# Performance work log

Hardware: AMD Instinct MI355X
Metric: run time of the kernel (lower is better)

## Reference

```python
import jax, jax.numpy as jnp
import numpy as np

ALPHA = 2.0  # snntorch ATan surrogate default (irrelevant for fwd-only)


def _spike(x):
    return (x > 0).astype(x.dtype)


def setup_inputs() -> dict:
    key = jax.random.key(0)
    ks = jax.random.split(key, 7)
    B, T, H, O = 2048, 120, 512, 2
    sample_rate = 40.0
    x = jax.random.normal(ks[0], (B, T), dtype=jnp.float32)
    # fc1: [H, 1], fc2: [O, H] (torch Linear weight layout), gaussian init near 1/sample_rate scale
    W1 = (1.0 / sample_rate) + (0.5 / sample_rate) * jax.random.normal(ks[1], (H, 1), dtype=jnp.float32)
    W2 = (1.0 / (sample_rate * H)) + (0.5 / (sample_rate * H)) * jax.random.normal(ks[2], (O, H), dtype=jnp.float32)
    W2 = W2 * H  # keep output currents at a useful magnitude
    beta_h = 0.8 + 0.19 * jax.random.uniform(ks[3], (H,), dtype=jnp.float32)
    thr_h = 1.0 + 0.1 * jax.random.uniform(ks[4], (H,), dtype=jnp.float32)
    beta_o = 0.8 + 0.19 * jax.random.uniform(ks[5], (O,), dtype=jnp.float32)
    thr_o = 1.0 + 0.1 * jax.random.uniform(ks[6], (O,), dtype=jnp.float32)
    return {"x": x, "W1": W1, "W2": W2, "beta_h": beta_h, "thr_h": thr_h,
            "beta_o": beta_o, "thr_o": thr_o}


def reference(x, W1, W2, beta_h, thr_h, beta_o, thr_o):
    B = x.shape[0]
    H, O = W1.shape[0], W2.shape[0]
    bh = jnp.clip(beta_h, 0.0, 1.0)
    bo = jnp.clip(beta_o, 0.0, 1.0)
    w1 = W1[:, 0]  # [H]; fc1 on scalar input is an outer product

    def step(carry, x_t):
        mem1, mem2 = carry
        cur1 = x_t[:, None] * w1[None, :]              # [B, H]
        mem1 = bh * mem1 + cur1
        spk1 = _spike(mem1 - thr_h)
        mem1 = mem1 * (1.0 - spk1)                      # zero reset, no delay
        cur2 = spk1 @ W2.T                              # [B, O]
        mem2 = bo * mem2 + cur2
        spk2 = _spike(mem2 - thr_o)
        mem2 = mem2 * (1.0 - spk2)
        return (mem1, mem2), (spk1, mem1, spk2, mem2)

    init = (jnp.zeros((B, H), x.dtype), jnp.zeros((B, O), x.dtype))
    xT = x.T  # [T, B] so scan walks time steps
    _, (spk1_rec, mem1_rec, spk2_rec, mem2_rec) = jax.lax.scan(step, init, xT)
    hidden_spike_count = spk1_rec.sum()
    output_spike_count = spk2_rec.sum()
    return spk1_rec, mem1_rec, spk2_rec, mem2_rec, hidden_spike_count, output_spike_count
```

## Files before the change

### kernel.cpp

```cpp
#include <hip/hip_runtime.h>

#define T_STEPS 120
#define BATCH   2048
#define HID     512
#define OUTN    2

#define SPK1_OFF 0LL
#define MEM1_OFF 125829120LL
#define SPK2_OFF 251658240LL
#define MEM2_OFF 252149760LL
#define CNT_OFF  252641280LL

__global__ void zero_counts_kernel(float* cnts) {
    cnts[0] = 0.0f;
    cnts[1] = 0.0f;
}

__global__ __launch_bounds__(512) void snn_fwd_kernel(
    const float* __restrict__ x,
    const float* __restrict__ W1,
    const float* __restrict__ W2,
    const float* __restrict__ beta_h,
    const float* __restrict__ thr_h,
    const float* __restrict__ beta_o,
    const float* __restrict__ thr_o,
    float* __restrict__ spk1_rec,
    float* __restrict__ mem1_rec,
    float* __restrict__ spk2_rec,
    float* __restrict__ mem2_rec,
    float* __restrict__ cnts)
{
    const int h = threadIdx.x;
    const int b = blockIdx.x;
    const int wid  = h >> 6;
    const int lane = h & 63;

    __shared__ float xs[T_STEPS];
    __shared__ float red[8][2];
    __shared__ float redc[8];

    if (h < T_STEPS) xs[h] = x[b * T_STEPS + h];

    const float w1 = W1[h];
    const float bh = fminf(fmaxf(beta_h[h], 0.0f), 1.0f);
    const float th = thr_h[h];
    const float w20 = W2[h];
    const float w21 = W2[HID + h];

    float bo0 = 0.f, bo1 = 0.f, to0 = 0.f, to1 = 0.f;
    if (h == 0) {
        bo0 = fminf(fmaxf(beta_o[0], 0.0f), 1.0f);
        bo1 = fminf(fmaxf(beta_o[1], 0.0f), 1.0f);
        to0 = thr_o[0];
        to1 = thr_o[1];
    }

    float m1 = 0.0f;
    float m2_0 = 0.0f, m2_1 = 0.0f;
    int hc = 0;
    int oc = 0;

    __syncthreads();

    for (int t = 0; t < T_STEPS; ++t) {
        const float xt = xs[t];
        m1 = __fadd_rn(__fmul_rn(bh, m1), __fmul_rn(xt, w1));
        const bool fired = (m1 > th);
        const float spk = fired ? 1.0f : 0.0f;
        if (fired) { m1 = 0.0f; hc++; }

        const long long idx1 = (long long)t * (BATCH * HID) + (long long)b * HID + h;
        spk1_rec[idx1] = spk;
        mem1_rec[idx1] = m1;

        float c0 = spk * w20;
        float c1 = spk * w21;
        if (__ballot(fired) != 0ULL) {
            for (int off = 32; off > 0; off >>= 1) {
                c0 += __shfl_down(c0, off, 64);
                c1 += __shfl_down(c1, off, 64);
            }
        }
        if (lane == 0) { red[wid][0] = c0; red[wid][1] = c1; }
        __syncthreads();

        if (h == 0) {
            float cur0 = 0.0f, cur1 = 0.0f;
            #pragma unroll
            for (int w = 0; w < 8; ++w) { cur0 += red[w][0]; cur1 += red[w][1]; }
            m2_0 = __fadd_rn(__fmul_rn(bo0, m2_0), cur0);
            m2_1 = __fadd_rn(__fmul_rn(bo1, m2_1), cur1);
            const bool f0 = (m2_0 > to0);
            const bool f1 = (m2_1 > to1);
            const float s0 = f0 ? 1.0f : 0.0f;
            const float s1 = f1 ? 1.0f : 0.0f;
            if (f0) { m2_0 = 0.0f; oc++; }
            if (f1) { m2_1 = 0.0f; oc++; }
            const long long idx2 = (long long)t * (BATCH * OUTN) + (long long)b * OUTN;
            spk2_rec[idx2]     = s0;
            spk2_rec[idx2 + 1] = s1;
            mem2_rec[idx2]     = m2_0;
            mem2_rec[idx2 + 1] = m2_1;
        }
        __syncthreads();
    }

    float fc = (float)hc;
    for (int off = 32; off > 0; off >>= 1) fc += __shfl_down(fc, off, 64);
    if (lane == 0) redc[wid] = fc;
    __syncthreads();
    if (h == 0) {
        float tot = 0.0f;
        #pragma unroll
        for (int w = 0; w < 8; ++w) tot += redc[w];
        atomicAdd(&cnts[0], tot);
        atomicAdd(&cnts[1], (float)oc);
    }
}

extern "C" void kernel_launch(void* const* d_in, const int* in_sizes, int n_in,
                              void* d_out, int out_size, void* d_ws, size_t ws_size,
                              hipStream_t stream) {
    const float* x      = (const float*)d_in[0];
    const float* W1     = (const float*)d_in[1];
    const float* W2     = (const float*)d_in[2];
    const float* beta_h = (const float*)d_in[3];
    const float* thr_h  = (const float*)d_in[4];
    const float* beta_o = (const float*)d_in[5];
    const float* thr_o  = (const float*)d_in[6];

    float* out  = (float*)d_out;
    float* spk1 = out + SPK1_OFF;
    float* mem1 = out + MEM1_OFF;
    float* spk2 = out + SPK2_OFF;
    float* mem2 = out + MEM2_OFF;
    float* cnts = out + CNT_OFF;

    zero_counts_kernel<<<1, 1, 0, stream>>>(cnts);

    snn_fwd_kernel<<<BATCH, HID, 0, stream>>>(
        x, W1, W2, beta_h, thr_h, beta_o, thr_o,
        spk1, mem1, spk2, mem2, cnts);
}
```

Measured before the change: 1.025 ms.

## Vectorize hidden neurons per thread and defer output layer past time loop

Each thread now handles four hidden neurons with float4 nontemporal stores, and blocks shrink from 512 to 128 threads. Per-step wave partial sums for the output layer go into a per-timestep shared array, so the two per-step block barriers are removed. The output-neuron recurrence is then run by two threads after the loop. The aim is to cut barrier stalls and store instruction count on a write-bandwidth-bound kernel, at the cost of a short serial tail and more shared memory.

After: 1.034 ms. About the same (+1.0%).

```diff
diff --git a/kernel.cpp b/kernel.cpp
--- a/kernel.cpp
+++ b/kernel.cpp
@@ -11,12 +11,14 @@
 #define MEM2_OFF 252149760LL
 #define CNT_OFF  252641280LL
 
+typedef float f32x4 __attribute__((ext_vector_type(4)));
+
 __global__ void zero_counts_kernel(float* cnts) {
     cnts[0] = 0.0f;
     cnts[1] = 0.0f;
 }
 
-__global__ __launch_bounds__(512) void snn_fwd_kernel(
+__global__ __launch_bounds__(128) void snn_fwd_kernel(
     const float* __restrict__ x,
     const float* __restrict__ W1,
     const float* __restrict__ W2,
@@ -30,91 +32,112 @@
     float* __restrict__ mem2_rec,
     float* __restrict__ cnts)
 {
-    const int h = threadIdx.x;
-    const int b = blockIdx.x;
-    const int wid  = h >> 6;
-    const int lane = h & 63;
+    const int tid  = threadIdx.x;
+    const int b    = blockIdx.x;
+    const int wid  = tid >> 6;
+    const int lane = tid & 63;
 
     __shared__ float xs[T_STEPS];
-    __shared__ float red[8][2];
-    __shared__ float redc[8];
+    __shared__ float red[T_STEPS][2][2];
+    __shared__ float redc[2];
 
-    if (h < T_STEPS) xs[h] = x[b * T_STEPS + h];
-
-    const float w1 = W1[h];
-    const float bh = fminf(fmaxf(beta_h[h], 0.0f), 1.0f);
-    const float th = thr_h[h];
-    const float w20 = W2[h];
-    const float w21 = W2[HID + h];
-
-    float bo0 = 0.f, bo1 = 0.f, to0 = 0.f, to1 = 0.f;
-    if (h == 0) {
-        bo0 = fminf(fmaxf(beta_o[0], 0.0f), 1.0f);
-        bo1 = fminf(fmaxf(beta_o[1], 0.0f), 1.0f);
-        to0 = thr_o[0];
-        to1 = thr_o[1];
+    if (tid < T_STEPS) {
+        ((f32x4*)red)[tid] = (f32x4)0.0f;
+        xs[tid] = x[(size_t)b * T_STEPS + tid];
     }
 
-    float m1 = 0.0f;
-    float m2_0 = 0.0f, m2_1 = 0.0f;
+    const f32x4 w1v  = ((const f32x4*)W1)[tid];
+    f32x4 bhv        = ((const f32x4*)beta_h)[tid];
+    const f32x4 thv  = ((const f32x4*)thr_h)[tid];
+    const f32x4 w20v = ((const f32x4*)W2)[tid];
+    const f32x4 w21v = ((const f32x4*)(W2 + HID))[tid];
+    bhv.x = fminf(fmaxf(bhv.x, 0.0f), 1.0f);
+    bhv.y = fminf(fmaxf(bhv.y, 0.0f), 1.0f);
+    bhv.z = fminf(fmaxf(bhv.z, 0.0f), 1.0f);
+    bhv.w = fminf(fmaxf(bhv.w, 0.0f), 1.0f);
+
+    float m0 = 0.0f, m1 = 0.0f, m2 = 0.0f, m3 = 0.0f;
     int hc = 0;
-    int oc = 0;
 
     __syncthreads();
 
+    const size_t off1    = (size_t)b * HID + (size_t)tid * 4;
+    const size_t stride1 = (size_t)BATCH * HID;
+    float* sp = spk1_rec + off1;
+    float* mp = mem1_rec + off1;
+
+    #pragma unroll 4
     for (int t = 0; t < T_STEPS; ++t) {
         const float xt = xs[t];
-        m1 = __fadd_rn(__fmul_rn(bh, m1), __fmul_rn(xt, w1));
-        const bool fired = (m1 > th);
-        const float spk = fired ? 1.0f : 0.0f;
-        if (fired) { m1 = 0.0f; hc++; }
+        m0 = __fadd_rn(__fmul_rn(bhv.x, m0), __fmul_rn(xt, w1v.x));
+        m1 = __fadd_rn(__fmul_rn(bhv.y, m1), __fmul_rn(xt, w1v.y));
+        m2 = __fadd_rn(__fmul_rn(bhv.z, m2), __fmul_rn(xt, w1v.z));
+        m3 = __fadd_rn(__fmul_rn(bhv.w, m3), __fmul_rn(xt, w1v.w));
 
-        const long long idx1 = (long long)t * (BATCH * HID) + (long long)b * HID + h;
-        spk1_rec[idx1] = spk;
-        mem1_rec[idx1] = m1;
+        const bool f0 = m0 > thv.x;
+        const bool f1 = m1 > thv.y;
+        const bool f2 = m2 > thv.z;
+        const bool f3 = m3 > thv.w;
+        const float s0 = f0 ? 1.0f : 0.0f;
+        const float s1 = f1 ? 1.0f : 0.0f;
+        const float s2 = f2 ? 1.0f : 0.0f;
+        const float s3 = f3 ? 1.0f : 0.0f;
+        m0 = f0 ? 0.0f : m0;
+        m1 = f1 ? 0.0f : m1;
+        m2 = f2 ? 0.0f : m2;
+        m3 = f3 ? 0.0f : m3;
+        hc += (int)f0 + (int)f1 + (int)f2 + (int)f3;
 
-        float c0 = spk * w20;
-        float c1 = spk * w21;
-        if (__ballot(fired) != 0ULL) {
-            for (int off = 32; off > 0; off >>= 1) {
-                c0 += __shfl_down(c0, off, 64);
-                c1 += __shfl_down(c1, off, 64);
+        f32x4 sv; sv.x = s0; sv.y = s1; sv.z = s2; sv.w = s3;
+        f32x4 mv; mv.x = m0; mv.y = m1; mv.z = m2; mv.w = m3;
+        __builtin_nontemporal_store(sv, (f32x4*)sp);
+        __builtin_nontemporal_store(mv, (f32x4*)mp);
+        sp += stride1;
+        mp += stride1;
+
+        if (__ballot(f0 | f1 | f2 | f3) != 0ULL) {
+            float c0 = s0 * w20v.x + s1 * w20v.y + s2 * w20v.z + s3 * w20v.w;
+            float c1 = s0 * w21v.x + s1 * w21v.y + s2 * w21v.z + s3 * w21v.w;
+            #pragma unroll
+            for (int o = 32; o > 0; o >>= 1) {
+                c0 += __shfl_down(c0, o, 64);
+                c1 += __shfl_down(c1, o, 64);
             }
+            if (lane == 0) { red[t][wid][0] = c0; red[t][wid][1] = c1; }
         }
-        if (lane == 0) { red[wid][0] = c0; red[wid][1] = c1; }
-        __syncthreads();
-
-        if (h == 0) {
-            float cur0 = 0.0f, cur1 = 0.0f;
-            #pragma unroll
-            for (int w = 0; w < 8; ++w) { cur0 += red[w][0]; cur1 += red[w][1]; }
-            m2_0 = __fadd_rn(__fmul_rn(bo0, m2_0), cur0);
-            m2_1 = __fadd_rn(__fmul_rn(bo1, m2_1), cur1);
-            const bool f0 = (m2_0 > to0);
-            const bool f1 = (m2_1 > to1);
-            const float s0 = f0 ? 1.0f : 0.0f;
-            const float s1 = f1 ? 1.0f : 0.0f;
-            if (f0) { m2_0 = 0.0f; oc++; }
-            if (f1) { m2_1 = 0.0f; oc++; }
-            const long long idx2 = (long long)t * (BATCH * OUTN) + (long long)b * OUTN;
-            spk2_rec[idx2]     = s0;
-            spk2_rec[idx2 + 1] = s1;
-            mem2_rec[idx2]     = m2_0;
-            mem2_rec[idx2 + 1] = m2_1;
-        }
-        __syncthreads();
     }
 
     float fc = (float)hc;
-    for (int off = 32; off > 0; off >>= 1) fc += __shfl_down(fc, off, 64);
+    #pragma unroll
+    for (int o = 32; o > 0; o >>= 1) fc += __shfl_down(fc, o, 64);
     if (lane == 0) redc[wid] = fc;
+
     __syncthreads();
-    if (h == 0) {
-        float tot = 0.0f;
-        #pragma unroll
-        for (int w = 0; w < 8; ++w) tot += redc[w];
-        atomicAdd(&cnts[0], tot);
-        atomicAdd(&cnts[1], (float)oc);
+
+    if (tid == 0) atomicAdd(&cnts[0], redc[0] + redc[1]);
+
+    if (tid < OUTN) {
+        const int o = tid;
+        const float bo = fminf(fmaxf(beta_o[o], 0.0f), 1.0f);
+        const float to = thr_o[o];
+        float m = 0.0f;
+        int oc = 0;
+        const size_t stride2 = (size_t)BATCH * OUTN;
+        float* s2p = spk2_rec + (size_t)b * OUTN + o;
+        float* m2p = mem2_rec + (size_t)b * OUTN + o;
+        #pragma unroll 4
+        for (int t = 0; t < T_STEPS; ++t) {
+            const float cur = red[t][0][o] + red[t][1][o];
+            m = __fadd_rn(__fmul_rn(bo, m), cur);
+            const bool f = m > to;
+            const float s = f ? 1.0f : 0.0f;
+            if (f) { m = 0.0f; oc++; }
+            s2p[0] = s;
+            m2p[0] = m;
+            s2p += stride2;
+            m2p += stride2;
+        }
+        if (oc) atomicAdd(&cnts[1], (float)oc);
     }
 }
 
@@ -138,7 +161,7 @@
 
     zero_counts_kernel<<<1, 1, 0, stream>>>(cnts);
 
-    snn_fwd_kernel<<<BATCH, HID, 0, stream>>>(
+    snn_fwd_kernel<<<BATCH, 128, 0, stream>>>(
         x, W1, W2, beta_h, thr_h, beta_o, thr_o,
         spk1, mem1, spk2, mem2, cnts);
 }
```
